# Optimization experiments

Hardware: AMD Instinct MI355X
Metric: run time of the kernel (lower is better)

## Reference

```python
import jax, jax.numpy as jnp
import numpy as np

B, CQ, CV, H, W, K = 8, 128, 64, 192, 192, 4


def conv3x3(x, w, b):
    # x [B,Cin,H,W], w [Cout,Cin,3,3], b [Cout]
    y = jax.lax.conv_general_dilated(
        x, w, window_strides=(1, 1), padding=((1, 1), (1, 1)),
        dimension_numbers=('NCHW', 'OIHW', 'NCHW'))
    return y + b[None, :, None, None]


def bilinear_sample(v, px, py):
    # v [B,C,H,W]; px,py [B,Ho,Wo] in pixel coords; zeros padding, align_corners=True
    Bv, C, Hv, Wv = v.shape
    x0 = jnp.floor(px); y0 = jnp.floor(py)
    x1 = x0 + 1.0;      y1 = y0 + 1.0
    wx1 = px - x0; wx0 = 1.0 - wx1
    wy1 = py - y0; wy0 = 1.0 - wy1
    vf = v.reshape(Bv, C, Hv * Wv)

    def gather(xi, yi):
        valid = (xi >= 0) & (xi <= Wv - 1) & (yi >= 0) & (yi <= Hv - 1)
        xc = jnp.clip(xi, 0, Wv - 1).astype(jnp.int32)
        yc = jnp.clip(yi, 0, Hv - 1).astype(jnp.int32)
        idx = (yc * Wv + xc).reshape(Bv, 1, -1)                # [B,1,Ho*Wo]
        vals = jnp.take_along_axis(vf, idx, axis=2)           # [B,C,Ho*Wo]
        vals = vals.reshape(Bv, C, *xi.shape[1:])
        return vals * valid[:, None].astype(v.dtype)

    out = (gather(x0, y0) * (wx0 * wy0)[:, None]
           + gather(x1, y0) * (wx1 * wy0)[:, None]
           + gather(x0, y1) * (wx0 * wy1)[:, None]
           + gather(x1, y1) * (wx1 * wy1)[:, None])
    return out


def setup_inputs() -> dict:
    key = jax.random.key(0)
    ks = jax.random.split(key, 10)
    s = 0.05
    return {
        'q': jax.random.normal(ks[0], (B, CQ, H, W), jnp.float32),
        'v': jax.random.normal(ks[1], (B, CV, H, W), jnp.float32),
        'ow1': jax.random.normal(ks[2], (CQ // 2, CQ, 3, 3), jnp.float32) * s,
        'ob1': jax.random.normal(ks[3], (CQ // 2,), jnp.float32) * s,
        'ow2': jax.random.normal(ks[4], (2 * K, CQ // 2, 3, 3), jnp.float32) * s,
        'ob2': jax.random.normal(ks[5], (2 * K,), jnp.float32) * s,
        'ww1': jax.random.normal(ks[6], (CQ // 2, CQ, 3, 3), jnp.float32) * s,
        'wb1': jax.random.normal(ks[7], (CQ // 2,), jnp.float32) * s,
        'ww2': jax.random.normal(ks[8], (K, CQ // 2, 3, 3), jnp.float32) * s,
        'wb2': jax.random.normal(ks[9], (K,), jnp.float32) * s,
    }


def reference(q, v, ow1, ob1, ow2, ob2, ww1, wb1, ww2, wb2):
    # offsets [B,2K,H,W], attention logits [B,K,H,W]
    offsets = conv3x3(jax.nn.gelu(conv3x3(q, ow1, ob1), approximate=False), ow2, ob2)
    logits = conv3x3(jax.nn.gelu(conv3x3(q, ww1, wb1), approximate=False), ww2, wb2)
    weights = jax.nn.softmax(logits, axis=1)                   # [B,K,H,W]

    xg = jnp.linspace(-1.0, 1.0, W, dtype=q.dtype)             # align_corners=True grid
    yg = jnp.linspace(-1.0, 1.0, H, dtype=q.dtype)
    base_x = jnp.broadcast_to(xg[None, :], (H, W))
    base_y = jnp.broadcast_to(yg[:, None], (H, W))

    off = offsets.reshape(B, K, 2, H, W)
    gx = base_x[None, None] + off[:, :, 0]                     # [B,K,H,W] normalized x
    gy = base_y[None, None] + off[:, :, 1]                     # [B,K,H,W] normalized y
    px = (gx + 1.0) * 0.5 * (W - 1)                            # pixel coords
    py = (gy + 1.0) * 0.5 * (H - 1)

    # vmap bilinear gather over the K sampling points -> [B,K,C,H,W]
    samp = jax.vmap(bilinear_sample, in_axes=(None, 1, 1), out_axes=1)(v, px, py)
    out = jnp.einsum('bkchw,bkhw->bchw', samp, weights)
    return out
```

## Files before the change

kernel.cpp:

```cpp
#include <hip/hip_runtime.h>
#include <hip/hip_bf16.h>
#include <cmath>

#define HH 192
#define WW 192
#define HWSZ (192*192)
#define NCQ 128
#define NCV 64
#define PP 194

typedef __attribute__((ext_vector_type(8))) short short8;
typedef __attribute__((ext_vector_type(4))) float f32x4;

__device__ inline uint16_t f2bf(float x){ __hip_bfloat16 h = __float2bfloat16(x); return *(uint16_t*)&h; }
__device__ inline float bf2f(uint16_t u){ return __uint_as_float(((uint32_t)u)<<16); }

__global__ __launch_bounds__(256) void k0z(uint16_t* __restrict__ qhi, uint16_t* __restrict__ qlo){
    int bi = blockIdx.x; int b = bi / PP; int yP = bi - b * PP;
    size_t rowbase = (((size_t)b * PP + yP) * PP) * NCQ;
    uint32_t* h32 = (uint32_t*)(qhi + rowbase);
    uint32_t* l32 = (uint32_t*)(qlo + rowbase);
    if (yP == 0 || yP == PP-1){
        for (int i = threadIdx.x; i < PP*NCQ/2; i += 256){ h32[i] = 0; l32[i] = 0; }
    } else {
        if (threadIdx.x < 64){ h32[threadIdx.x] = 0; l32[threadIdx.x] = 0; }
        else if (threadIdx.x < 128){ int i = (PP-1)*64 + threadIdx.x - 64; h32[i] = 0; l32[i] = 0; }
    }
}

__global__ __launch_bounds__(256) void k0w(const float* __restrict__ ow1, const float* __restrict__ ww1,
                                           uint16_t* __restrict__ whi, uint16_t* __restrict__ wlo){
    int d = blockIdx.x * 256 + threadIdx.x;
    if (d >= 128 * 1152) return;
    int m = d / 1152; int r = d - m * 1152; int tap = r >> 7; int ic = r & 127;
    float wv = (m < 64) ? ow1[((size_t)m * NCQ + ic) * 9 + tap]
                        : ww1[((size_t)(m - 64) * NCQ + ic) * 9 + tap];
    uint16_t hi = f2bf(wv);
    uint16_t lo = f2bf(wv - bf2f(hi));
    whi[d] = hi; wlo[d] = lo;
}

__global__ __launch_bounds__(256) void k0q(const float* __restrict__ q,
                                           uint16_t* __restrict__ qhi, uint16_t* __restrict__ qlo){
    __shared__ uint16_t lh[64 * 136], ll[64 * 136];
    const int x0 = blockIdx.x * 64, y = blockIdx.y, b = blockIdx.z;
    const int t = threadIdx.x;
    const int xr = t & 63;
#pragma unroll 4
    for (int it = 0; it < 32; ++it){
        int ic = it * 4 + (t >> 6);
        float val = q[(((size_t)b * NCQ + ic) * HH + y) * WW + x0 + xr];
        uint16_t hi = f2bf(val);
        uint16_t lo = f2bf(val - bf2f(hi));
        lh[xr * 136 + ic] = hi;
        ll[xr * 136 + ic] = lo;
    }
    __syncthreads();
#pragma unroll
    for (int it = 0; it < 4; ++it){
        int s = t + it * 256;
        int x = s >> 4, icb = (s & 15) * 8;
        size_t dst = (((size_t)b * PP + y + 1) * PP + (x0 + x + 1)) * NCQ + icb;
        *(int4*)(qhi + dst) = *(const int4*)(lh + x * 136 + icb);
        *(int4*)(qlo + dst) = *(const int4*)(ll + x * 136 + icb);
    }
}

__global__ __launch_bounds__(256) void k1_conv1_mfma(
    const uint16_t* __restrict__ qhi, const uint16_t* __restrict__ qlo,
    const uint16_t* __restrict__ whi, const uint16_t* __restrict__ wlo,
    const float* __restrict__ ob1, const float* __restrict__ wb1,
    float* __restrict__ t1)
{
    __shared__ uint16_t qlds[2 * 6336];
    const int tid = threadIdx.x;
    const int b = blockIdx.y;
    const int strip = blockIdx.x % 3;
    const int y = blockIdx.x / 3;
    const int x0 = strip * 64;
    const int lane = tid & 63;
    const int wid = tid >> 6;
    const int wm = wid >> 1;
    const int wn = wid & 1;
    const int l15 = lane & 15;
    const int g = lane >> 4;

    const uint16_t* ssrc[7]; int slds[7]; bool sok[7];
#pragma unroll
    for (int j = 0; j < 7; ++j){
        int s = tid + j * 256;
        sok[j] = (s < 1584);
        int p = (s >= 792) ? 1 : 0;
        int s7 = s - p * 792;
        int r = s7 / 264;
        int tt = s7 - r * 264;
        int c = tt >> 2;
        int t3 = tt & 3;
        const uint16_t* base = p ? qlo : qhi;
        ssrc[j] = base + (((size_t)b * PP + y + r) * PP + (x0 + c)) * NCQ + t3 * 8;
        slds[j] = p * 6336 + s7 * 8;
    }

    f32x4 acc[4][2];
#pragma unroll
    for (int mf = 0; mf < 4; ++mf)
#pragma unroll
        for (int nf = 0; nf < 2; ++nf) acc[mf][nf] = (f32x4){0.f,0.f,0.f,0.f};

    float4 sreg[7];
#pragma unroll
    for (int j = 0; j < 7; ++j) if (sok[j]) sreg[j] = *(const float4*)(ssrc[j]);

    for (int kc = 0; kc < 4; ++kc){
        __syncthreads();
#pragma unroll
        for (int j = 0; j < 7; ++j) if (sok[j]) *(float4*)(&qlds[slds[j]]) = sreg[j];
        __syncthreads();
        if (kc < 3){
#pragma unroll
            for (int j = 0; j < 7; ++j) if (sok[j]) sreg[j] = *(const float4*)(ssrc[j] + (kc + 1) * 32);
        }
        const int kb = kc * 32;
#pragma unroll
        for (int dy = 0; dy < 3; ++dy)
#pragma unroll
        for (int dx = 0; dx < 3; ++dx){
            const int tap = dy * 3 + dx;
            short8 bh[2], bl[2];
#pragma unroll
            for (int nf = 0; nf < 2; ++nf){
                int c = wn * 32 + nf * 16 + l15 + dx;
                int off = (dy * 66 + c) * 32 + 8 * g;
                bh[nf] = *(const short8*)(&qlds[off]);
                bl[nf] = *(const short8*)(&qlds[6336 + off]);
            }
#pragma unroll
            for (int mf = 0; mf < 4; ++mf){
                size_t wo = (size_t)((wm * 64 + mf * 16 + l15) * 9 + tap) * 128 + kb + 8 * g;
                short8 ah = *(const short8*)(whi + wo);
                short8 al = *(const short8*)(wlo + wo);
#pragma unroll
                for (int nf = 0; nf < 2; ++nf){
                    acc[mf][nf] = __builtin_amdgcn_mfma_f32_16x16x32_bf16(ah, bh[nf], acc[mf][nf], 0, 0, 0);
                    acc[mf][nf] = __builtin_amdgcn_mfma_f32_16x16x32_bf16(ah, bl[nf], acc[mf][nf], 0, 0, 0);
                    acc[mf][nf] = __builtin_amdgcn_mfma_f32_16x16x32_bf16(al, bh[nf], acc[mf][nf], 0, 0, 0);
                }
            }
        }
    }

    const float* bias = wm ? wb1 : ob1;
#pragma unroll
    for (int mf = 0; mf < 4; ++mf){
#pragma unroll
        for (int nf = 0; nf < 2; ++nf){
#pragma unroll
            for (int qq = 0; qq < 4; ++qq){
                int ocl = mf * 16 + g * 4 + qq;
                float xv = acc[mf][nf][qq] + bias[ocl];
                float ge = 0.5f * xv * (1.0f + erff(xv * 0.70710678118654752f));
                int oc = wm * 64 + ocl;
                int x = x0 + wn * 32 + nf * 16 + l15;
                t1[(((size_t)b * NCQ + oc) * HH + y) * WW + x] = ge;
            }
        }
    }
}

__global__ __launch_bounds__(256) void k2b_vcl(const float* __restrict__ v, uint16_t* __restrict__ vcl){
    __shared__ uint16_t tl[64 * 72];
    const int x0 = blockIdx.x * 64, y = blockIdx.y, b = blockIdx.z;
    const int t = threadIdx.x;
    const int xr = t & 63;
#pragma unroll 4
    for (int it = 0; it < 16; ++it){
        int c = it * 4 + (t >> 6);
        float val = v[(((size_t)b * NCV + c) * HH + y) * WW + x0 + xr];
        tl[xr * 72 + c] = f2bf(val);
    }
    __syncthreads();
#pragma unroll
    for (int it = 0; it < 2; ++it){
        int s = t + it * 256;
        int x = s >> 3, cb = (s & 7) * 8;
        size_t dst = ((size_t)b * HWSZ + (size_t)y * WW + x0 + x) * NCV + cb;
        *(int4*)(vcl + dst) = *(const int4*)(tl + x * 72 + cb);
    }
}

__global__ __launch_bounds__(256) void k2a_prep(
    const float* __restrict__ t1,
    const float* __restrict__ ow2, const float* __restrict__ ob2,
    const float* __restrict__ ww2, const float* __restrict__ wb2,
    float2* __restrict__ sparm)
{
    __shared__ float lds[16 * 360];
    const int tid = threadIdx.x;
    const int b   = blockIdx.y;
    const int ty0 = (blockIdx.x / 12) << 4;
    const int tx0 = (blockIdx.x % 12) << 4;

    int  sgoff[2], slds2[2];
    bool swr[2], sok2[2];
#pragma unroll
    for (int j = 0; j < 2; ++j){
        const int i = tid + j * 256;
        const int r = i / 18;
        const int c = i - r * 18;
        const int gy = ty0 - 1 + r;
        const int gx = tx0 - 1 + c;
        swr[j]   = (i < 324);
        sok2[j]  = swr[j] && (gy >= 0) && (gy < HH) && (gx >= 0) && (gx < WW);
        sgoff[j] = gy * WW + gx;
        slds2[j] = r * 20 + c;
    }
    const float* tb = t1 + (size_t)b * NCQ * HWSZ;

    float acc[12];
#pragma unroll
    for (int i = 0; i < 12; ++i) acc[i] = 0.f;

    const int ty = tid >> 4, tx = tid & 15;

    for (int cb = 0; cb < 64; cb += 8){
        __syncthreads();
#pragma unroll
        for (int p = 0; p < 16; ++p){
            const int ch = (p < 8) ? (cb + p) : (64 + cb + (p - 8));
            const float* tp = tb + (size_t)ch * HWSZ;
#pragma unroll
            for (int j = 0; j < 2; ++j)
                if (swr[j]) lds[p * 360 + slds2[j]] = sok2[j] ? tp[sgoff[j]] : 0.f;
        }
        __syncthreads();
#pragma unroll
        for (int p = 0; p < 8; ++p){
            float win[3][3];
#pragma unroll
            for (int r = 0; r < 3; ++r)
#pragma unroll
                for (int c = 0; c < 3; ++c)
                    win[r][c] = lds[p * 360 + (ty + r) * 20 + (tx + c)];
            const float* wo = ow2 + (cb + p) * 9;
#pragma unroll
            for (int oc = 0; oc < 8; ++oc)
#pragma unroll
                for (int t = 0; t < 9; ++t)
                    acc[oc] = fmaf(wo[oc * 576 + t], win[t / 3][t % 3], acc[oc]);

            float win2[3][3];
#pragma unroll
            for (int r = 0; r < 3; ++r)
#pragma unroll
                for (int c = 0; c < 3; ++c)
                    win2[r][c] = lds[(p + 8) * 360 + (ty + r) * 20 + (tx + c)];
            const float* wl = ww2 + (cb + p) * 9;
#pragma unroll
            for (int oc = 0; oc < 4; ++oc)
#pragma unroll
                for (int t = 0; t < 9; ++t)
                    acc[8 + oc] = fmaf(wl[oc * 576 + t], win2[t / 3][t % 3], acc[8 + oc]);
        }
    }

    const int y = ty0 + ty, x = tx0 + tx;

    float offv[8];
#pragma unroll
    for (int i = 0; i < 8; ++i) offv[i] = acc[i] + ob2[i];
    float lg[4];
#pragma unroll
    for (int i = 0; i < 4; ++i) lg[i] = acc[8 + i] + wb2[i];

    const float m = fmaxf(fmaxf(lg[0], lg[1]), fmaxf(lg[2], lg[3]));
    float e[4], s = 0.f;
#pragma unroll
    for (int i = 0; i < 4; ++i){ e[i] = expf(lg[i] - m); s += e[i]; }
    const float sinv = 1.f / s;

    float2 pr[16];
#pragma unroll
    for (int k = 0; k < 4; ++k){
        const float wk = e[k] * sinv;
        const float px = (float)x + offv[2 * k]     * (0.5f * (WW - 1));
        const float py = (float)y + offv[2 * k + 1] * (0.5f * (HH - 1));
        const float fx0 = floorf(px), fy0 = floorf(py);
        const float wx1 = px - fx0, wx0f = 1.f - wx1;
        const float wy1 = py - fy0, wy0f = 1.f - wy1;
#pragma unroll
        for (int cy = 0; cy < 2; ++cy)
#pragma unroll
            for (int cx = 0; cx < 2; ++cx){
                const float fx = fx0 + (float)cx;
                const float fy = fy0 + (float)cy;
                const bool ok = (fx >= 0.f) && (fx <= (float)(WW - 1)) &&
                                (fy >= 0.f) && (fy <= (float)(HH - 1));
                const int xi = (int)fminf(fmaxf(fx, 0.f), (float)(WW - 1));
                const int yi = (int)fminf(fmaxf(fy, 0.f), (float)(HH - 1));
                const float wgt = (cx ? wx1 : wx0f) * (cy ? wy1 : wy0f) * wk;
                pr[k * 4 + cy * 2 + cx] = make_float2(ok ? wgt : 0.f,
                                                      __int_as_float(yi * WW + xi));
            }
    }
    float2* sp = sparm + ((size_t)b * HWSZ + (size_t)y * WW + x) * 16;
#pragma unroll
    for (int i = 0; i < 16; ++i) sp[i] = pr[i];
}

__global__ __launch_bounds__(1024) void k3_gather(
    const float2* __restrict__ sparm, const uint16_t* __restrict__ vcl,
    float* __restrict__ out)
{
    const int tid = threadIdx.x;
    const int wid = tid >> 6, lane = tid & 63;
    const int p = blockIdx.x * 16 + wid;
    const int b = p / HWSZ;
    const int hw = p - b * HWSZ;
    (void)hw;

    const float4* s4 = (const float4*)(sparm + (size_t)p * 16);
    float4 f[8];
#pragma unroll
    for (int i = 0; i < 8; ++i) f[i] = s4[i];

    const uint16_t* vb = vcl + (size_t)b * HWSZ * NCV + lane;
    float acc = 0.f;
#pragma unroll
    for (int i = 0; i < 8; ++i){
        int i0 = __float_as_int(f[i].y);
        int i1 = __float_as_int(f[i].w);
        acc = fmaf(f[i].x, bf2f(vb[(size_t)i0 * NCV]), acc);
        acc = fmaf(f[i].z, bf2f(vb[(size_t)i1 * NCV]), acc);
    }

    __shared__ float tl[64 * 17];
    tl[lane * 17 + wid] = acc;
    __syncthreads();
    if (tid < 256){
        int c = tid >> 2, x4 = (tid & 3) * 4;
        int p0 = blockIdx.x * 16;
        int b0 = p0 / HWSZ; int hw0 = p0 - b0 * HWSZ;
        float4 o = make_float4(tl[c * 17 + x4], tl[c * 17 + x4 + 1],
                               tl[c * 17 + x4 + 2], tl[c * 17 + x4 + 3]);
        *(float4*)(out + ((size_t)b0 * NCV + c) * HWSZ + hw0 + x4) = o;
    }
}

extern "C" void kernel_launch(void* const* d_in, const int* in_sizes, int n_in,
                              void* d_out, int out_size, void* d_ws, size_t ws_size,
                              hipStream_t stream) {
    const float* q   = (const float*)d_in[0];
    const float* v   = (const float*)d_in[1];
    const float* ow1 = (const float*)d_in[2];
    const float* ob1 = (const float*)d_in[3];
    const float* ow2 = (const float*)d_in[4];
    const float* ob2 = (const float*)d_in[5];
    const float* ww1 = (const float*)d_in[6];
    const float* wb1 = (const float*)d_in[7];
    const float* ww2 = (const float*)d_in[8];
    const float* wb2 = (const float*)d_in[9];

    char* ws = (char*)d_ws;
    float*    t1   = (float*)ws;
    uint16_t* whi  = (uint16_t*)(ws + 150994944);
    uint16_t* wlo  = (uint16_t*)(ws + 150994944 + 294912);
    const size_t QOFF = 150994944 + 589824;
    const size_t QPL  = (size_t)8 * PP * PP * NCQ * 2;
    uint16_t* qhi  = (uint16_t*)(ws + QOFF);
    uint16_t* qlo  = (uint16_t*)(ws + QOFF + QPL);
    uint16_t* vcl  = (uint16_t*)(ws + QOFF);
    float2*  sparm = (float2*)  (ws + QOFF + 37748736);

    float* out = (float*)d_out;

    k0z<<<dim3(8 * PP), dim3(256), 0, stream>>>(qhi, qlo);
    k0w<<<dim3(576), dim3(256), 0, stream>>>(ow1, ww1, whi, wlo);
    k0q<<<dim3(3, 192, 8), dim3(256), 0, stream>>>(q, qhi, qlo);
    k1_conv1_mfma<<<dim3(576, 8), dim3(256), 0, stream>>>(qhi, qlo, whi, wlo, ob1, wb1, t1);
    k2b_vcl<<<dim3(3, 192, 8), dim3(256), 0, stream>>>(v, vcl);
    k2a_prep<<<dim3(144, 8), dim3(256), 0, stream>>>(t1, ow2, ob2, ww2, wb2, sparm);
    k3_gather<<<dim3(18432), dim3(1024), 0, stream>>>(sparm, vcl, out);
}
```

Measured before the change: 1.745 ms.

## Widen conv1 MFMA tile to 96 pixels and relayout weights per tap/k-chunk

The first 3x3 conv kernel now covers 96-pixel strips instead of 64, so each wave computes three N fragments rather than two. This reuses each loaded weight fragment across more pixels and cuts the halo overhead of the staged input rows. The weight split kernel also writes hi/lo weights in a [tap][kchunk][oc][32] layout, so a wave's A-fragment loads hit contiguous memory, and launch_bounds now requests 2 blocks per CU. In exchange the kernel uses more LDS and accumulator registers and launches fewer blocks, which could lower occupancy.

```diff
diff --git a/kernel.cpp b/kernel.cpp
--- a/kernel.cpp
+++ b/kernel.cpp
@@ -37,7 +37,8 @@
                         : ww1[((size_t)(m - 64) * NCQ + ic) * 9 + tap];
     uint16_t hi = f2bf(wv);
     uint16_t lo = f2bf(wv - bf2f(hi));
-    whi[d] = hi; wlo[d] = lo;
+    int dst = ((tap * 4 + (ic >> 5)) * 128 + m) * 32 + (ic & 31);
+    whi[dst] = hi; wlo[dst] = lo;
 }
 
 __global__ __launch_bounds__(256) void k0q(const float* __restrict__ q,
@@ -66,18 +67,18 @@
     }
 }
 
-__global__ __launch_bounds__(256) void k1_conv1_mfma(
+__global__ __launch_bounds__(256, 2) void k1_conv1_mfma(
     const uint16_t* __restrict__ qhi, const uint16_t* __restrict__ qlo,
     const uint16_t* __restrict__ whi, const uint16_t* __restrict__ wlo,
     const float* __restrict__ ob1, const float* __restrict__ wb1,
     float* __restrict__ t1)
 {
-    __shared__ uint16_t qlds[2 * 6336];
+    __shared__ uint16_t qlds[2 * 9408];
     const int tid = threadIdx.x;
     const int b = blockIdx.y;
-    const int strip = blockIdx.x % 3;
-    const int y = blockIdx.x / 3;
-    const int x0 = strip * 64;
+    const int strip = blockIdx.x & 1;
+    const int y = blockIdx.x >> 1;
+    const int x0 = strip * 96;
     const int lane = tid & 63;
     const int wid = tid >> 6;
     const int wm = wid >> 1;
@@ -85,62 +86,60 @@
     const int l15 = lane & 15;
     const int g = lane >> 4;
 
-    const uint16_t* ssrc[7]; int slds[7]; bool sok[7];
-#pragma unroll
-    for (int j = 0; j < 7; ++j){
+    const uint16_t* ssrc[10]; int slds[10]; bool sok[10];
+#pragma unroll
+    for (int j = 0; j < 10; ++j){
         int s = tid + j * 256;
-        sok[j] = (s < 1584);
-        int p = (s >= 792) ? 1 : 0;
-        int s7 = s - p * 792;
-        int r = s7 / 264;
-        int tt = s7 - r * 264;
-        int c = tt >> 2;
-        int t3 = tt & 3;
+        sok[j] = (s < 2352);
+        int ss = sok[j] ? s : 0;
+        int p = (ss >= 1176) ? 1 : 0;
+        int s2 = ss - p * 1176;
+        int r = s2 / 392;
+        int c2 = s2 - r * 392;
+        int c = c2 >> 2;
+        int t3 = c2 & 3;
         const uint16_t* base = p ? qlo : qhi;
         ssrc[j] = base + (((size_t)b * PP + y + r) * PP + (x0 + c)) * NCQ + t3 * 8;
-        slds[j] = p * 6336 + s7 * 8;
-    }
-
-    f32x4 acc[4][2];
+        slds[j] = s * 8;
+    }
+
+    f32x4 acc[4][3];
 #pragma unroll
     for (int mf = 0; mf < 4; ++mf)
 #pragma unroll
-        for (int nf = 0; nf < 2; ++nf) acc[mf][nf] = (f32x4){0.f,0.f,0.f,0.f};
-
-    float4 sreg[7];
-#pragma unroll
-    for (int j = 0; j < 7; ++j) if (sok[j]) sreg[j] = *(const float4*)(ssrc[j]);
+        for (int nf = 0; nf < 3; ++nf) acc[mf][nf] = (f32x4){0.f,0.f,0.f,0.f};
+
+    float4 sreg[10];
+#pragma unroll
+    for (int j = 0; j < 10; ++j) if (sok[j]) sreg[j] = *(const float4*)(ssrc[j]);
 
     for (int kc = 0; kc < 4; ++kc){
         __syncthreads();
 #pragma unroll
-        for (int j = 0; j < 7; ++j) if (sok[j]) *(float4*)(&qlds[slds[j]]) = sreg[j];
+        for (int j = 0; j < 10; ++j) if (sok[j]) *(float4*)(&qlds[slds[j]]) = sreg[j];
         __syncthreads();
         if (kc < 3){
 #pragma unroll
-            for (int j = 0; j < 7; ++j) if (sok[j]) sreg[j] = *(const float4*)(ssrc[j] + (kc + 1) * 32);
-        }
-        const int kb = kc * 32;
-#pragma unroll
-        for (int dy = 0; dy < 3; ++dy)
-#pragma unroll
-        for (int dx = 0; dx < 3; ++dx){
-            const int tap = dy * 3 + dx;
-            short8 bh[2], bl[2];
-#pragma unroll
-            for (int nf = 0; nf < 2; ++nf){
-                int c = wn * 32 + nf * 16 + l15 + dx;
-                int off = (dy * 66 + c) * 32 + 8 * g;
+            for (int j = 0; j < 10; ++j) if (sok[j]) sreg[j] = *(const float4*)(ssrc[j] + (kc + 1) * 32);
+        }
+#pragma unroll
+        for (int tap = 0; tap < 9; ++tap){
+            const int dy = tap / 3, dx = tap % 3;
+            short8 bh[3], bl[3];
+#pragma unroll
+            for (int nf = 0; nf < 3; ++nf){
+                int c = wn * 48 + nf * 16 + l15 + dx;
+                int off = (dy * 98 + c) * 32 + 8 * g;
                 bh[nf] = *(const short8*)(&qlds[off]);
-                bl[nf] = *(const short8*)(&qlds[6336 + off]);
+                bl[nf] = *(const short8*)(&qlds[9408 + off]);
             }
 #pragma unroll
             for (int mf = 0; mf < 4; ++mf){
-                size_t wo = (size_t)((wm * 64 + mf * 16 + l15) * 9 + tap) * 128 + kb + 8 * g;
+                size_t wo = ((size_t)(tap * 4 + kc) * 128 + wm * 64 + mf * 16 + l15) * 32 + 8 * g;
                 short8 ah = *(const short8*)(whi + wo);
                 short8 al = *(const short8*)(wlo + wo);
 #pragma unroll
-                for (int nf = 0; nf < 2; ++nf){
+                for (int nf = 0; nf < 3; ++nf){
                     acc[mf][nf] = __builtin_amdgcn_mfma_f32_16x16x32_bf16(ah, bh[nf], acc[mf][nf], 0, 0, 0);
                     acc[mf][nf] = __builtin_amdgcn_mfma_f32_16x16x32_bf16(ah, bl[nf], acc[mf][nf], 0, 0, 0);
                     acc[mf][nf] = __builtin_amdgcn_mfma_f32_16x16x32_bf16(al, bh[nf], acc[mf][nf], 0, 0, 0);
@@ -153,14 +152,14 @@
 #pragma unroll
     for (int mf = 0; mf < 4; ++mf){
 #pragma unroll
-        for (int nf = 0; nf < 2; ++nf){
+        for (int nf = 0; nf < 3; ++nf){
 #pragma unroll
             for (int qq = 0; qq < 4; ++qq){
                 int ocl = mf * 16 + g * 4 + qq;
                 float xv = acc[mf][nf][qq] + bias[ocl];
                 float ge = 0.5f * xv * (1.0f + erff(xv * 0.70710678118654752f));
                 int oc = wm * 64 + ocl;
-                int x = x0 + wn * 32 + nf * 16 + l15;
+                int x = x0 + wn * 48 + nf * 16 + l15;
                 t1[(((size_t)b * NCQ + oc) * HH + y) * WW + x] = ge;
             }
         }
@@ -315,8 +314,6 @@
     const int wid = tid >> 6, lane = tid & 63;
     const int p = blockIdx.x * 16 + wid;
     const int b = p / HWSZ;
-    const int hw = p - b * HWSZ;
-    (void)hw;
 
     const float4* s4 = (const float4*)(sparm + (size_t)p * 16);
     float4 f[8];
@@ -376,7 +373,7 @@
     k0z<<<dim3(8 * PP), dim3(256), 0, stream>>>(qhi, qlo);
     k0w<<<dim3(576), dim3(256), 0, stream>>>(ow1, ww1, whi, wlo);
     k0q<<<dim3(3, 192, 8), dim3(256), 0, stream>>>(q, qhi, qlo);
-    k1_conv1_mfma<<<dim3(576, 8), dim3(256), 0, stream>>>(qhi, qlo, whi, wlo, ob1, wb1, t1);
+    k1_conv1_mfma<<<dim3(384, 8), dim3(256), 0, stream>>>(qhi, qlo, whi, wlo, ob1, wb1, t1);
     k2b_vcl<<<dim3(3, 192, 8), dim3(256), 0, stream>>>(v, vcl);
     k2a_prep<<<dim3(144, 8), dim3(256), 0, stream>>>(t1, ow2, ob2, ww2, wb2, sparm);
     k3_gather<<<dim3(18432), dim3(1024), 0, stream>>>(sparm, vcl, out);
```

After: 1.540 ms. -11.7%, faster.
